# Performance work log

Hardware: AMD Instinct MI355X
Metric: run time of the kernel (lower is better)

## Reference

```python
import jax, jax.numpy as jnp
import numpy as np
from jax import lax

VOCAB = 50000   # marker token id == vocab_size
EMB = 1024
HID = 1024      # bidirectional total
HD = HID // 2   # per-direction hidden
LAYERS = 2
B, T = 32, 512


def setup_inputs() -> dict:
    key = jax.random.key(0)
    ks = jax.random.split(key, 12)
    seq = jax.random.randint(ks[0], (B, T), 1, VOCAB)
    pos = jax.random.randint(ks[1], (B,), 0, T)
    seq = seq.at[jnp.arange(B), pos].set(VOCAB)  # exactly one marker per row
    label = (jax.random.uniform(ks[2], (B,)) > 0.5).astype(jnp.float32)
    s = 1.0 / np.sqrt(HD)
    w_emb = jax.random.normal(ks[3], (VOCAB + 1, EMB), jnp.float32) * 0.05
    w_ih = jax.random.uniform(ks[4], (LAYERS, 2, 4 * HD, EMB), jnp.float32, -s, s)
    w_hh = jax.random.uniform(ks[5], (LAYERS, 2, 4 * HD, HD), jnp.float32, -s, s)
    b = jax.random.uniform(ks[6], (LAYERS, 2, 4 * HD), jnp.float32, -s, s)
    w1 = jax.random.normal(ks[7], (HD, HID), jnp.float32) * 0.03
    b1 = jnp.zeros((HD,), jnp.float32)
    w2 = jax.random.normal(ks[8], (1, HD), jnp.float32) * 0.03
    b2 = jnp.zeros((1,), jnp.float32)
    return {"seq": seq, "label": label, "w_emb": w_emb, "w_ih": w_ih,
            "w_hh": w_hh, "b": b, "w1": w1, "b1": b1, "w2": w2, "b2": b2}


def _run_dir(x, Wih, Whh, bb, reverse):
    # x: [B,T,In]; precompute input contribution to all 4 gates (i,f,g,o order, torch layout)
    gx = jnp.einsum('bti,gi->btg', x, Wih) + bb  # [B,T,4*HD]

    def step(carry, g):
        h, c = carry
        g = g + h @ Whh.T
        i, f, gg, o = jnp.split(g, 4, axis=-1)
        c = jax.nn.sigmoid(f) * c + jax.nn.sigmoid(i) * jnp.tanh(gg)
        h = jax.nn.sigmoid(o) * jnp.tanh(c)
        return (h, c), h

    h0 = jnp.zeros((x.shape[0], HD), x.dtype)
    _, hs = lax.scan(step, (h0, h0), gx.transpose(1, 0, 2), reverse=reverse)
    return hs.transpose(1, 0, 2)  # [B,T,HD], time order preserved


def reference(seq, label, w_emb, w_ih, w_hh, b, w1, b1, w2, b2):
    emb = w_emb.at[0].set(0.0)[seq]  # padding_idx=0 -> zero vector
    x = emb
    for l in range(LAYERS):
        fwd = _run_dir(x, w_ih[l, 0], w_hh[l, 0], b[l, 0], False)
        bwd = _run_dir(x, w_ih[l, 1], w_hh[l, 1], b[l, 1], True)
        x = jnp.concatenate([fwd, bwd], axis=-1)  # [B,T,HID]
    # masked_select at the single marker position per row -> [B,HID]
    idx = jnp.argmax(seq == VOCAB, axis=1)
    hidden = x[jnp.arange(x.shape[0]), idx]
    h = jnp.tanh(hidden @ w1.T + b1)
    logit = (h @ w2.T + b2)[:, 0]
    # BCEWithLogits, mean reduction: softplus(z) - z*y
    return jnp.mean(jax.nn.softplus(logit) - logit * label)
```

## Files before the change

### kernel.cpp

```cpp
#include <hip/hip_runtime.h>
#include <stdint.h>

typedef unsigned short u16;
typedef __bf16 bf16x8 __attribute__((ext_vector_type(8)));
typedef float  f32x4  __attribute__((ext_vector_type(4)));

#define GPTR(p) ((const __attribute__((address_space(1))) void*)(p))
#define LPTR(p) ((__attribute__((address_space(3))) void*)(p))

__device__ __forceinline__ u16 f2bf(float f) {
  uint32_t u = __float_as_uint(f);
  u += 0x7FFFu + ((u >> 16) & 1u);
  return (u16)(u >> 16);
}
__device__ __forceinline__ float bf2f(u16 h) {
  return __uint_as_float(((uint32_t)h) << 16);
}
__device__ __forceinline__ float sigf(float x) { return 1.0f / (1.0f + __expf(-x)); }
__device__ __forceinline__ float tanhf_(float x) { return 1.0f - 2.0f / (__expf(2.0f * x) + 1.0f); }

__global__ void k_emb(const int* __restrict__ seq, const float* __restrict__ wemb,
                      u16* __restrict__ x1) {
  const int row = blockIdx.x;
  const int tok = seq[row];
  float4 v = ((const float4*)(wemb + (size_t)tok * 1024))[threadIdx.x];
  uint32_t lo = (uint32_t)f2bf(v.x) | ((uint32_t)f2bf(v.y) << 16);
  uint32_t hi = (uint32_t)f2bf(v.z) | ((uint32_t)f2bf(v.w) << 16);
  *(uint2*)(x1 + (size_t)row * 1024 + threadIdx.x * 4) = make_uint2(lo, hi);
}

__global__ void k_idx(const int* __restrict__ seq, int* __restrict__ idxb) {
  const int tid = threadIdx.x;
  const int b = tid >> 3, part = tid & 7;
  for (int t = part * 64; t < part * 64 + 64; ++t)
    if (seq[b * 512 + t] == 50000) idxb[b] = t;
}

__global__ void k_cast(const float* __restrict__ src, u16* __restrict__ dst) {
  const int i = blockIdx.x * 256 + threadIdx.x;
  float4 v = ((const float4*)src)[i];
  uint32_t lo = (uint32_t)f2bf(v.x) | ((uint32_t)f2bf(v.y) << 16);
  uint32_t hi = (uint32_t)f2bf(v.z) | ((uint32_t)f2bf(v.w) << 16);
  *(uint2*)(dst + (size_t)i * 4) = make_uint2(lo, hi);
}

__global__ __launch_bounds__(256) void k_gemm(
    const u16* __restrict__ X, const u16* __restrict__ W,
    const float* __restrict__ bias, u16* __restrict__ gx)
{
  __shared__ u16 As[128][32];
  __shared__ u16 Bs[128][32];
  const int tid = threadIdx.x;
  const int lane = tid & 63;
  const int wv = tid >> 6;
  const int wm = wv >> 1, wn = wv & 1;
  const int bm = blockIdx.x, bn = blockIdx.y;
  const int srow = tid >> 2;
  const int scg = (tid & 3) * 8;
  const u16* Xb = X + (size_t)bm * 128 * 1024;
  const u16* Wb = W + (size_t)bn * 128 * 1024;
  f32x4 acc[4][4] = {};
  for (int k0 = 0; k0 < 1024; k0 += 32) {
    __builtin_amdgcn_global_load_lds(GPTR(Xb + (size_t)srow * 1024 + k0 + scg),        LPTR(&As[srow][scg]),       16, 0, 0);
    __builtin_amdgcn_global_load_lds(GPTR(Xb + (size_t)(srow + 64) * 1024 + k0 + scg), LPTR(&As[srow + 64][scg]), 16, 0, 0);
    __builtin_amdgcn_global_load_lds(GPTR(Wb + (size_t)srow * 1024 + k0 + scg),        LPTR(&Bs[srow][scg]),       16, 0, 0);
    __builtin_amdgcn_global_load_lds(GPTR(Wb + (size_t)(srow + 64) * 1024 + k0 + scg), LPTR(&Bs[srow + 64][scg]), 16, 0, 0);
    __syncthreads();
    const int kg = (lane >> 4) * 8;
    bf16x8 a4[4], b4[4];
    #pragma unroll
    for (int mt = 0; mt < 4; ++mt) a4[mt] = *(const bf16x8*)&As[wm * 64 + mt * 16 + (lane & 15)][kg];
    #pragma unroll
    for (int nt = 0; nt < 4; ++nt) b4[nt] = *(const bf16x8*)&Bs[wn * 64 + nt * 16 + (lane & 15)][kg];
    #pragma unroll
    for (int mt = 0; mt < 4; ++mt)
      #pragma unroll
      for (int nt = 0; nt < 4; ++nt)
        acc[mt][nt] = __builtin_amdgcn_mfma_f32_16x16x32_bf16(a4[mt], b4[nt], acc[mt][nt], 0, 0, 0);
    __syncthreads();
  }
  #pragma unroll
  for (int mt = 0; mt < 4; ++mt) {
    const int mbase = bm * 128 + wm * 64 + mt * 16 + ((lane >> 4) << 2);
    #pragma unroll
    for (int nt = 0; nt < 4; ++nt) {
      const int n = bn * 128 + wn * 64 + nt * 16 + (lane & 15);
      const float bi = bias[n];
      const int d = n >> 11;
      const int nn = n & 2047;
      const int q = nn >> 9;
      const int j = nn & 511;
      const int col = (j >> 4) * 64 + q * 16 + (j & 15);
      #pragma unroll
      for (int r = 0; r < 4; ++r) {
        const int mm = mbase + r;
        const int b = mm >> 9, t = mm & 511;
        gx[((size_t)(d * 512 + t) * 32 + b) * 2048 + col] = f2bf(acc[mt][nt][r] + bi);
      }
    }
  }
}

__global__ __launch_bounds__(256, 1) void k_rec(
    const u16* __restrict__ gx, const float* __restrict__ whh,
    u16* __restrict__ xout, u16* hstep)
{
  const int bid = blockIdx.x;
  const int dir = bid >> 5;
  const int db = bid & 31;
  const int j0 = db * 16;
  const int tid = threadIdx.x;
  const int lane = tid & 63;
  const int wv = tid >> 6;
  const int mh = wv >> 1, nh = wv & 1;
  const int R = lane & 15;
  const int ks = lane >> 4;

  __shared__ float G[2][32][68];

  bf16x8 bw[2][16];
  {
    #pragma unroll
    for (int nt = 0; nt < 2; ++nt) {
      const int q = nh * 2 + nt;
      const float* wp = whh + ((size_t)dir * 2048 + q * 512 + j0 + R) * 512 + ks * 8;
      #pragma unroll
      for (int kt = 0; kt < 16; ++kt) {
        float4 v0 = *(const float4*)(wp + kt * 32);
        float4 v1 = *(const float4*)(wp + kt * 32 + 4);
        union { u16 u[8]; bf16x8 v; } t;
        t.u[0] = f2bf(v0.x); t.u[1] = f2bf(v0.y); t.u[2] = f2bf(v0.z); t.u[3] = f2bf(v0.w);
        t.u[4] = f2bf(v1.x); t.u[5] = f2bf(v1.y); t.u[6] = f2bf(v1.z); t.u[7] = f2bf(v1.w);
        bw[nt][kt] = t.v;
      }
    }
  }

  const int eb = tid >> 3;
  const int pr = (tid & 7) * 2;
  float c0 = 0.f, c1 = 0.f;

  const size_t dirbase = (size_t)dir * 512 * 16384;
  const u16* apbase = hstep + dirbase + (size_t)(ks >> 1) * 512 + (mh * 16 + R) * 16 + (ks & 1) * 8;
  const u16* prbase = hstep + dirbase + (size_t)(lane & 31) * 512 + 510;
  const u16* gxeb   = gx + ((size_t)dir * 512 * 32 + eb) * 2048 + db * 64 + pr;

  uint32_t gq[4];
  {
    const int t0 = dir ? 511 : 0;
    const uint32_t* g0 = (const uint32_t*)(gxeb + (size_t)t0 * 65536);
    gq[0] = g0[0]; gq[1] = g0[8]; gq[2] = g0[16]; gq[3] = g0[24];
  }

  for (int s = 0; s < 512; ++s) {
    const int tcur = dir ? (511 - s) : s;
    const int gb = s & 1;
    f32x4 acc0 = {0.f,0.f,0.f,0.f}, acc1 = {0.f,0.f,0.f,0.f};

    if (s) {
      const size_t slot = (size_t)(s - 1) * 16384;
      const u16* ap = apbase + slot;
      {
        const u16* pp = prbase + slot;
        while (true) {
          uint32_t fv;
          asm volatile("global_load_dword %0, %1, off sc0 sc1\n\ts_waitcnt vmcnt(0)"
                       : "=v"(fv) : "v"(pp) : "memory");
          if (__all((int)(fv != 0xFFFFFFFFu))) break;
        }
      }
      __builtin_amdgcn_sched_barrier(0);
      uint4 afu[16];
      #pragma unroll
      for (int kt = 0; kt < 16; ++kt)
        asm volatile("global_load_dwordx4 %0, %1, off sc0 sc1"
                     : "=v"(afu[kt]) : "v"(ap + kt * 1024) : "memory");
      asm volatile("s_waitcnt vmcnt(8)" ::: "memory");
      __builtin_amdgcn_sched_barrier(0);
      while (true) {
        unsigned mask = 0;
        #pragma unroll
        for (int kt = 0; kt < 8; ++kt) {
          int ok = (afu[kt].x != 0xFFFFFFFFu) && (afu[kt].y != 0xFFFFFFFFu) &&
                   (afu[kt].z != 0xFFFFFFFFu) && (afu[kt].w != 0xFFFFFFFFu);
          if (!__all(ok)) mask |= 1u << kt;
        }
        if (!mask) break;
        #pragma unroll
        for (int kt = 0; kt < 8; ++kt)
          if (mask & (1u << kt))
            asm volatile("global_load_dwordx4 %0, %1, off sc0 sc1"
                         : "=v"(afu[kt]) : "v"(ap + kt * 1024) : "memory");
        asm volatile("s_waitcnt vmcnt(0)" ::: "memory");
        __builtin_amdgcn_sched_barrier(0);
      }
      f32x4 a0 = {0.f,0.f,0.f,0.f}, a1 = {0.f,0.f,0.f,0.f};
      f32x4 b0 = {0.f,0.f,0.f,0.f}, b1 = {0.f,0.f,0.f,0.f};
      #pragma unroll
      for (int kt = 0; kt < 8; kt += 2) {
        bf16x8 x = __builtin_bit_cast(bf16x8, afu[kt]);
        bf16x8 y = __builtin_bit_cast(bf16x8, afu[kt + 1]);
        a0 = __builtin_amdgcn_mfma_f32_16x16x32_bf16(x, bw[0][kt],     a0, 0, 0, 0);
        a1 = __builtin_amdgcn_mfma_f32_16x16x32_bf16(x, bw[1][kt],     a1, 0, 0, 0);
        b0 = __builtin_amdgcn_mfma_f32_16x16x32_bf16(y, bw[0][kt + 1], b0, 0, 0, 0);
        b1 = __builtin_amdgcn_mfma_f32_16x16x32_bf16(y, bw[1][kt + 1], b1, 0, 0, 0);
      }
      asm volatile("s_waitcnt vmcnt(0)" ::: "memory");
      __builtin_amdgcn_sched_barrier(0);
      while (true) {
        unsigned mask = 0;
        #pragma unroll
        for (int kt = 8; kt < 16; ++kt) {
          int ok = (afu[kt].x != 0xFFFFFFFFu) && (afu[kt].y != 0xFFFFFFFFu) &&
                   (afu[kt].z != 0xFFFFFFFFu) && (afu[kt].w != 0xFFFFFFFFu);
          if (!__all(ok)) mask |= 1u << (kt - 8);
        }
        if (!mask) break;
        #pragma unroll
        for (int kt = 8; kt < 16; ++kt)
          if (mask & (1u << (kt - 8)))
            asm volatile("global_load_dwordx4 %0, %1, off sc0 sc1"
                         : "=v"(afu[kt]) : "v"(ap + kt * 1024) : "memory");
        asm volatile("s_waitcnt vmcnt(0)" ::: "memory");
        __builtin_amdgcn_sched_barrier(0);
      }
      #pragma unroll
      for (int kt = 8; kt < 16; kt += 2) {
        bf16x8 x = __builtin_bit_cast(bf16x8, afu[kt]);
        bf16x8 y = __builtin_bit_cast(bf16x8, afu[kt + 1]);
        a0 = __builtin_amdgcn_mfma_f32_16x16x32_bf16(x, bw[0][kt],     a0, 0, 0, 0);
        a1 = __builtin_amdgcn_mfma_f32_16x16x32_bf16(x, bw[1][kt],     a1, 0, 0, 0);
        b0 = __builtin_amdgcn_mfma_f32_16x16x32_bf16(y, bw[0][kt + 1], b0, 0, 0, 0);
        b1 = __builtin_amdgcn_mfma_f32_16x16x32_bf16(y, bw[1][kt + 1], b1, 0, 0, 0);
      }
      acc0 = a0 + b0;
      acc1 = a1 + b1;
    }

    #pragma unroll
    for (int r = 0; r < 4; ++r) {
      G[gb][mh * 16 + (lane >> 4) * 4 + r][nh * 32 + (lane & 15)]      = acc0[r];
      G[gb][mh * 16 + (lane >> 4) * 4 + r][nh * 32 + 16 + (lane & 15)] = acc1[r];
    }
    __syncthreads();

    {
      float i0 = G[gb][eb][pr]      + bf2f((u16)(gq[0] & 0xFFFF));
      float i1 = G[gb][eb][pr + 1]  + bf2f((u16)(gq[0] >> 16));
      float f0 = G[gb][eb][pr + 16] + bf2f((u16)(gq[1] & 0xFFFF));
      float f1 = G[gb][eb][pr + 17] + bf2f((u16)(gq[1] >> 16));
      float g0 = G[gb][eb][pr + 32] + bf2f((u16)(gq[2] & 0xFFFF));
      float g1 = G[gb][eb][pr + 33] + bf2f((u16)(gq[2] >> 16));
      float o0 = G[gb][eb][pr + 48] + bf2f((u16)(gq[3] & 0xFFFF));
      float o1 = G[gb][eb][pr + 49] + bf2f((u16)(gq[3] >> 16));
      c0 = sigf(f0) * c0 + sigf(i0) * tanhf_(g0);
      c1 = sigf(f1) * c1 + sigf(i1) * tanhf_(g1);
      float h0 = sigf(o0) * tanhf_(c0);
      float h1 = sigf(o1) * tanhf_(c1);
      uint32_t hp = (uint32_t)f2bf(h0) | ((uint32_t)f2bf(h1) << 16);
      u16* hdst = hstep + dirbase + (size_t)s * 16384 + (size_t)db * 512 + eb * 16 + pr;
      asm volatile("global_store_dword %0, %1, off sc0 sc1"
                   :: "v"(hdst), "v"(hp) : "memory");
      *(uint32_t*)(xout + ((size_t)eb * 512 + tcur) * 1024 + dir * 512 + j0 + pr) = hp;
    }
    if (s < 511) {
      const int tn = dir ? (511 - (s + 1)) : (s + 1);
      const uint32_t* gn = (const uint32_t*)(gxeb + (size_t)tn * 65536);
      gq[0] = gn[0]; gq[1] = gn[8]; gq[2] = gn[16]; gq[3] = gn[24];
    }
  }
}

__global__ void k_cls1(const u16* __restrict__ x3, const int* __restrict__ idxb,
                       const float* __restrict__ w1, const float* __restrict__ b1,
                       float* __restrict__ h1) {
  __shared__ u16 hid[32][1024];
  const int tid = threadIdx.x;
  for (int g = tid; g < 4096; g += 256) {
    const int b = g >> 7;
    const int c8 = (g & 127) * 8;
    *(uint4*)&hid[b][c8] = *(const uint4*)(x3 + ((size_t)b * 512 + idxb[b]) * 1024 + c8);
  }
  __syncthreads();
  for (int p = tid; p < 1024; p += 256) {
    const int j = blockIdx.x * 32 + (p >> 5);
    const int b = p & 31;
    const float4* wr = (const float4*)(w1 + (size_t)j * 1024);
    float s = 0.f;
    for (int k4 = 0; k4 < 256; ++k4) {
      float4 wv = wr[k4];
      const int k = k4 * 4;
      s += bf2f(hid[b][k]) * wv.x + bf2f(hid[b][k + 1]) * wv.y
         + bf2f(hid[b][k + 2]) * wv.z + bf2f(hid[b][k + 3]) * wv.w;
    }
    h1[b * 512 + j] = tanhf_(s + b1[j]);
  }
}

__global__ void k_cls2(const float* __restrict__ h1, const float* __restrict__ w2,
                       const float* __restrict__ b2, const float* __restrict__ label,
                       float* __restrict__ out) {
  const int lane = threadIdx.x;
  float loss = 0.f;
  for (int b = 0; b < 32; ++b) {
    float s = 0.f;
    for (int k = lane; k < 512; k += 64) s += h1[b * 512 + k] * w2[k];
    for (int off = 32; off; off >>= 1) s += __shfl_down(s, off);
    if (lane == 0) {
      const float z = s + b2[0];
      const float y = label[b];
      const float sp = fmaxf(z, 0.f) + log1pf(__expf(-fabsf(z)));
      loss += sp - z * y;
    }
  }
  if (lane == 0) out[0] = loss / 32.0f;
}

extern "C" void kernel_launch(void* const* d_in, const int* in_sizes, int n_in,
                              void* d_out, int out_size, void* d_ws, size_t ws_size,
                              hipStream_t stream) {
  const int*   seq   = (const int*)  d_in[0];
  const float* label = (const float*)d_in[1];
  const float* wemb  = (const float*)d_in[2];
  const float* wih   = (const float*)d_in[3];
  const float* whh   = (const float*)d_in[4];
  const float* bb    = (const float*)d_in[5];
  const float* w1    = (const float*)d_in[6];
  const float* b1    = (const float*)d_in[7];
  const float* w2    = (const float*)d_in[8];
  const float* b2    = (const float*)d_in[9];

  u16* x1   = (u16*)d_ws;
  u16* x2   = x1 + (size_t)16777216;
  u16* gxb  = x2 + (size_t)16777216;
  u16* wb   = gxb + (size_t)67108864;
  float* h1 = (float*)(wb + 4194304);
  int* idxb = (int*)(h1 + 16384);

  k_emb<<<16384, 256, 0, stream>>>(seq, wemb, x1);
  k_idx<<<1, 256, 0, stream>>>(seq, idxb);
  k_cast<<<4096, 256, 0, stream>>>(wih, wb);
  k_gemm<<<dim3(128, 32), 256, 0, stream>>>(x1, wb, bb, gxb);
  hipMemsetAsync(x1, 0xFF, (size_t)33554432, stream);
  k_rec<<<64, 256, 0, stream>>>(gxb, whh, x2, x1);
  k_cast<<<4096, 256, 0, stream>>>(wih + 4194304, wb);
  k_gemm<<<dim3(128, 32), 256, 0, stream>>>(x2, wb, bb + 4096, gxb);
  hipMemsetAsync(x2, 0xFF, (size_t)33554432, stream);
  k_rec<<<64, 256, 0, stream>>>(gxb, whh + 2097152, x1, x2);
  k_cls1<<<16, 256, 0, stream>>>(x1, idxb, w1, b1, h1);
  k_cls2<<<1, 64, 0, stream>>>(h1, w2, b2, label, (float*)d_out);
}
```

Before: 4.063 ms.

## Use per-block step flags for recurrence sync and overlap gate prefetch with h loads

Blocks in the cross-block recurrence no longer spin on a sentinel word inside the hidden-state buffer. Instead each block's last thread writes a dedicated per-step completion flag, and consumers poll a compact flag array that is zeroed by an extra memset. The next step's precomputed gate-input loads are issued alongside the hidden-state loads, with the vmcnt waits adjusted, so their latency overlaps the MFMA work instead of trailing the step. The flag is stored without a block barrier, so it can become visible before other waves' h stores. The existing sentinel retry loops still catch any stale data, at the cost of possible extra reloads.

```diff
diff --git a/kernel.cpp b/kernel.cpp
--- a/kernel.cpp
+++ b/kernel.cpp
@@ -103,7 +103,7 @@
 
 __global__ __launch_bounds__(256, 1) void k_rec(
     const u16* __restrict__ gx, const float* __restrict__ whh,
-    u16* __restrict__ xout, u16* hstep)
+    u16* __restrict__ xout, u16* hstep, unsigned* flags)
 {
   const int bid = blockIdx.x;
   const int dir = bid >> 5;
@@ -142,8 +142,8 @@
 
   const size_t dirbase = (size_t)dir * 512 * 16384;
   const u16* apbase = hstep + dirbase + (size_t)(ks >> 1) * 512 + (mh * 16 + R) * 16 + (ks & 1) * 8;
-  const u16* prbase = hstep + dirbase + (size_t)(lane & 31) * 512 + 510;
-  const u16* gxeb   = gx + ((size_t)dir * 512 * 32 + eb) * 2048 + db * 64 + pr;
+  const unsigned* flbase = flags + dir * 16384 + (lane & 31);
+  const u16* gxeb = gx + ((size_t)dir * 512 * 32 + eb) * 2048 + db * 64 + pr;
 
   uint32_t gq[4];
   {
@@ -156,17 +156,18 @@
     const int tcur = dir ? (511 - s) : s;
     const int gb = s & 1;
     f32x4 acc0 = {0.f,0.f,0.f,0.f}, acc1 = {0.f,0.f,0.f,0.f};
+    uint32_t gqn[4];
 
     if (s) {
       const size_t slot = (size_t)(s - 1) * 16384;
       const u16* ap = apbase + slot;
       {
-        const u16* pp = prbase + slot;
+        const unsigned* fp = flbase + (s - 1) * 32;
         while (true) {
           uint32_t fv;
           asm volatile("global_load_dword %0, %1, off sc0 sc1\n\ts_waitcnt vmcnt(0)"
-                       : "=v"(fv) : "v"(pp) : "memory");
-          if (__all((int)(fv != 0xFFFFFFFFu))) break;
+                       : "=v"(fv) : "v"(fp) : "memory");
+          if (__all((int)(fv != 0u))) break;
         }
       }
       __builtin_amdgcn_sched_barrier(0);
@@ -175,7 +176,12 @@
       for (int kt = 0; kt < 16; ++kt)
         asm volatile("global_load_dwordx4 %0, %1, off sc0 sc1"
                      : "=v"(afu[kt]) : "v"(ap + kt * 1024) : "memory");
-      asm volatile("s_waitcnt vmcnt(8)" ::: "memory");
+      if (s < 511) {
+        const int tn = dir ? (511 - (s + 1)) : (s + 1);
+        const uint32_t* gn = (const uint32_t*)(gxeb + (size_t)tn * 65536);
+        gqn[0] = gn[0]; gqn[1] = gn[8]; gqn[2] = gn[16]; gqn[3] = gn[24];
+      }
+      asm volatile("s_waitcnt vmcnt(12)" ::: "memory");
       __builtin_amdgcn_sched_barrier(0);
       while (true) {
         unsigned mask = 0;
@@ -205,7 +211,7 @@
         b0 = __builtin_amdgcn_mfma_f32_16x16x32_bf16(y, bw[0][kt + 1], b0, 0, 0, 0);
         b1 = __builtin_amdgcn_mfma_f32_16x16x32_bf16(y, bw[1][kt + 1], b1, 0, 0, 0);
       }
-      asm volatile("s_waitcnt vmcnt(0)" ::: "memory");
+      asm volatile("s_waitcnt vmcnt(4)" ::: "memory");
       __builtin_amdgcn_sched_barrier(0);
       while (true) {
         unsigned mask = 0;
@@ -235,6 +241,10 @@
       }
       acc0 = a0 + b0;
       acc1 = a1 + b1;
+    } else {
+      const int tn = dir ? 510 : 1;
+      const uint32_t* gn = (const uint32_t*)(gxeb + (size_t)tn * 65536);
+      gqn[0] = gn[0]; gqn[1] = gn[8]; gqn[2] = gn[16]; gqn[3] = gn[24];
     }
 
     #pragma unroll
@@ -262,11 +272,15 @@
       asm volatile("global_store_dword %0, %1, off sc0 sc1"
                    :: "v"(hdst), "v"(hp) : "memory");
       *(uint32_t*)(xout + ((size_t)eb * 512 + tcur) * 1024 + dir * 512 + j0 + pr) = hp;
+      if (tid == 255) {
+        unsigned one = 1u;
+        unsigned* fdst = flags + dir * 16384 + s * 32 + db;
+        asm volatile("global_store_dword %0, %1, off sc0 sc1"
+                     :: "v"(fdst), "v"(one) : "memory");
+      }
     }
     if (s < 511) {
-      const int tn = dir ? (511 - (s + 1)) : (s + 1);
-      const uint32_t* gn = (const uint32_t*)(gxeb + (size_t)tn * 65536);
-      gq[0] = gn[0]; gq[1] = gn[8]; gq[2] = gn[16]; gq[3] = gn[24];
+      gq[0] = gqn[0]; gq[1] = gqn[1]; gq[2] = gqn[2]; gq[3] = gqn[3];
     }
   }
 }
@@ -336,17 +350,20 @@
   u16* wb   = gxb + (size_t)67108864;
   float* h1 = (float*)(wb + 4194304);
   int* idxb = (int*)(h1 + 16384);
-
+  unsigned* fl1 = (unsigned*)(idxb + 32);
+  unsigned* fl2 = fl1 + 32768;
+
+  hipMemsetAsync(fl1, 0, 262144, stream);
   k_emb<<<16384, 256, 0, stream>>>(seq, wemb, x1);
   k_idx<<<1, 256, 0, stream>>>(seq, idxb);
   k_cast<<<4096, 256, 0, stream>>>(wih, wb);
   k_gemm<<<dim3(128, 32), 256, 0, stream>>>(x1, wb, bb, gxb);
   hipMemsetAsync(x1, 0xFF, (size_t)33554432, stream);
-  k_rec<<<64, 256, 0, stream>>>(gxb, whh, x2, x1);
+  k_rec<<<64, 256, 0, stream>>>(gxb, whh, x2, x1, fl1);
   k_cast<<<4096, 256, 0, stream>>>(wih + 4194304, wb);
   k_gemm<<<dim3(128, 32), 256, 0, stream>>>(x2, wb, bb + 4096, gxb);
   hipMemsetAsync(x2, 0xFF, (size_t)33554432, stream);
-  k_rec<<<64, 256, 0, stream>>>(gxb, whh + 2097152, x1, x2);
+  k_rec<<<64, 256, 0, stream>>>(gxb, whh + 2097152, x1, x2, fl2);
   k_cls1<<<16, 256, 0, stream>>>(x1, idxb, w1, b1, h1);
   k_cls2<<<1, 64, 0, stream>>>(h1, w2, b2, label, (float*)d_out);
 }
```

Result: slower. 4.193 ms (+3.2%).
